# Kernel tuning notes

Hardware: AMD Instinct MI355X
Metric: run time of the kernel (lower is better)

Reference implementation:

```python
import jax, jax.numpy as jnp
import numpy as np

GRID = (128, 128, 128)
NUM_EMB = GRID[0] * GRID[1] * GRID[2]
EMB_DIM = 32
N_PTS = 2097152


def setup_inputs() -> dict:
    key = jax.random.key(0)
    k1, k2 = jax.random.split(key)
    # points uniform in the unit bounding box [0,1)^3
    x = jax.random.uniform(k1, (N_PTS, 3), dtype=jnp.float32)
    emb = jax.random.normal(k2, (NUM_EMB, EMB_DIM), dtype=jnp.float32)
    return {"x": x, "emb": emb}


def reference(x, emb):
    gx, gy, gz = GRID
    box_min = jnp.zeros((3,), jnp.float32)
    # scale_factor = grid_size / (box_max - box_min); box = [0,1]^3
    scale = jnp.array([gx, gy, gz], jnp.float32)
    xr = (x - box_min) * scale          # [N,3]
    x_idx = jnp.floor(xr)
    xw = xr - x_idx                      # trilinear weights, [N,3]

    c000 = (x_idx[:, 0] + x_idx[:, 1] * gx + x_idx[:, 2] * gx * gy).astype(jnp.int32)
    c001 = c000 + 1
    c010 = c000 + gx
    c100 = c000 + gx * gy
    c011 = c000 + gx + 1
    c101 = c000 + gx * gy + 1
    c110 = c000 + gx * gy + gx
    c111 = c000 + gx * gy + gx + 1

    # boundary clamping exactly as in the torch module
    c000 = jnp.where(c000 >= NUM_EMB, NUM_EMB - 1, c000)
    clamp = lambda c: jnp.where(c >= NUM_EMB, c000, c)
    c001, c010, c100 = clamp(c001), clamp(c010), clamp(c100)
    c011, c101, c110, c111 = clamp(c011), clamp(c101), clamp(c110), clamp(c111)

    # 8 gathers: [8, N, D]
    idx = jnp.stack([c000, c001, c010, c100, c011, c101, c110, c111])
    v = emb[idx]
    v000, v001, v010, v100, v011, v101, v110, v111 = v

    xw0 = xw[:, 0:1]
    xw1 = xw[:, 1:2]
    xw2 = xw[:, 2:3]
    c00 = v000 * (1 - xw0) + v100 * xw0
    c01 = v001 * (1 - xw0) + v101 * xw0
    c10 = v010 * (1 - xw0) + v110 * xw0
    c11 = v011 * (1 - xw0) + v111 * xw0
    c0 = c00 * (1 - xw1) + c10 * xw1
    c1 = c01 * (1 - xw1) + c11 * xw1
    return c0 * (1 - xw2) + c1 * xw2     # [N, D]
```

## Files before the change

kernel.cpp:

```cpp
#include <hip/hip_runtime.h>

#define GX 128
#define NUM_EMB (GX * GX * GX)

__global__ __launch_bounds__(256) void grid_emb_kernel(
    const float* __restrict__ x,
    const float4* __restrict__ emb4,
    float4* __restrict__ out4,
    int n_pts)
{
    int tid = blockIdx.x * 256 + threadIdx.x;
    int p = tid >> 3;
    int g = tid & 7;
    if (p >= n_pts) return;

    float xr0 = x[3 * p + 0] * (float)GX;
    float xr1 = x[3 * p + 1] * (float)GX;
    float xr2 = x[3 * p + 2] * (float)GX;
    float f0 = floorf(xr0), f1 = floorf(xr1), f2 = floorf(xr2);
    float w0 = xr0 - f0, w1 = xr1 - f1, w2 = xr2 - f2;

    int c000 = (int)f0 + (int)f1 * GX + (int)f2 * (GX * GX);
    if (c000 >= NUM_EMB) c000 = NUM_EMB - 1;

    int c[8];
    c[0] = c000;
    c[1] = c000 + 1;
    c[2] = c000 + GX;
    c[3] = c000 + GX * GX;
    c[4] = c000 + GX + 1;
    c[5] = c000 + GX * GX + 1;
    c[6] = c000 + GX * GX + GX;
    c[7] = c000 + GX * GX + GX + 1;
#pragma unroll
    for (int k = 1; k < 8; ++k) c[k] = (c[k] >= NUM_EMB) ? c000 : c[k];

    float m0 = 1.f - w0, m1 = 1.f - w1, m2 = 1.f - w2;
    float wt[8];
    wt[0] = m0 * m1 * m2;
    wt[1] = m0 * m1 * w2;
    wt[2] = m0 * w1 * m2;
    wt[3] = w0 * m1 * m2;
    wt[4] = m0 * w1 * w2;
    wt[5] = w0 * m1 * w2;
    wt[6] = w0 * w1 * m2;
    wt[7] = w0 * w1 * w2;

    float4 v[8];
#pragma unroll
    for (int k = 0; k < 8; ++k) v[k] = emb4[c[k] * 8 + g];

    float4 acc;
    acc.x = 0.f; acc.y = 0.f; acc.z = 0.f; acc.w = 0.f;
#pragma unroll
    for (int k = 0; k < 8; ++k) {
        acc.x = fmaf(wt[k], v[k].x, acc.x);
        acc.y = fmaf(wt[k], v[k].y, acc.y);
        acc.z = fmaf(wt[k], v[k].z, acc.z);
        acc.w = fmaf(wt[k], v[k].w, acc.w);
    }

    out4[p * 8 + g] = acc;
}

extern "C" void kernel_launch(void* const* d_in, const int* in_sizes, int n_in,
                              void* d_out, int out_size, void* d_ws, size_t ws_size,
                              hipStream_t stream) {
    const float* x = (const float*)d_in[0];
    const float4* emb4 = (const float4*)d_in[1];
    float4* out4 = (float4*)d_out;

    int n_pts = in_sizes[0] / 3;
    int total_threads = n_pts * 8;
    int blocks = (total_threads + 255) / 256;
    grid_emb_kernel<<<blocks, 256, 0, stream>>>(x, emb4, out4, n_pts);
}
```

Before: 684.2 us.

## Counting-sort points by grid row before trilinear gather for cache locality

Adds a histogram, scan and scatter pipeline that buckets points by their (y,z) grid row. The main kernel then processes points in that bucket order through an index indirection. Neighbouring threads gather nearby embedding rows, which should raise cache hit rates on the 256MB table that random gathers were thrashing. In exchange it adds four extra launches, atomic contention on the buckets, and scattered output writes.

```diff
diff --git a/kernel.cpp b/kernel.cpp
--- a/kernel.cpp
+++ b/kernel.cpp
@@ -2,17 +2,75 @@
 
 #define GX 128
 #define NUM_EMB (GX * GX * GX)
+#define NBUCKETS 16384
 
-__global__ __launch_bounds__(256) void grid_emb_kernel(
+
+__device__ __forceinline__ int cell_of(const float* __restrict__ x, int p) {
+    float xr0 = x[3 * p + 0] * (float)GX;
+    float xr1 = x[3 * p + 1] * (float)GX;
+    float xr2 = x[3 * p + 2] * (float)GX;
+    int i0 = (int)floorf(xr0);
+    int i1 = (int)floorf(xr1);
+    int i2 = (int)floorf(xr2);
+    int c = i0 + (i1 << 7) + (i2 << 14);
+    if (c >= NUM_EMB) c = NUM_EMB - 1;
+    return c;
+}
+
+__global__ void zero_hist_kernel(unsigned* __restrict__ hist) {
+    int i = blockIdx.x * 256 + threadIdx.x;
+    if (i < NBUCKETS) hist[i] = 0u;
+}
+
+__global__ void hist_kernel(const float* __restrict__ x, unsigned* __restrict__ hist, int n) {
+    int p = blockIdx.x * 256 + threadIdx.x;
+    if (p >= n) return;
+    atomicAdd(&hist[cell_of(x, p) >> 7], 1u);
+}
+
+__global__ __launch_bounds__(1024) void scan_kernel(unsigned* __restrict__ hist) {
+    __shared__ unsigned part[1024];
+    unsigned t = threadIdx.x;
+    unsigned base = t * 16;
+    unsigned v[16];
+    unsigned s = 0;
+#pragma unroll
+    for (int i = 0; i < 16; ++i) { v[i] = hist[base + i]; s += v[i]; }
+    part[t] = s;
+    __syncthreads();
+    for (int off = 1; off < 1024; off <<= 1) {
+        unsigned cur = part[t];
+        unsigned add = (t >= (unsigned)off) ? part[t - off] : 0u;
+        __syncthreads();
+        part[t] = cur + add;
+        __syncthreads();
+    }
+    unsigned excl = (t == 0) ? 0u : part[t - 1];
+#pragma unroll
+    for (int i = 0; i < 16; ++i) { unsigned tmp = v[i]; hist[base + i] = excl; excl += tmp; }
+}
+
+__global__ void scatter_kernel(const float* __restrict__ x, unsigned* __restrict__ cursors,
+                               unsigned* __restrict__ sorted, int n) {
+    int p = blockIdx.x * 256 + threadIdx.x;
+    if (p >= n) return;
+    unsigned b = (unsigned)(cell_of(x, p) >> 7);
+    unsigned pos = atomicAdd(&cursors[b], 1u);
+    sorted[pos] = (unsigned)p;
+}
+
+__global__ __launch_bounds__(256) void grid_emb_main_kernel(
     const float* __restrict__ x,
     const float4* __restrict__ emb4,
+    const unsigned* __restrict__ sorted,
     float4* __restrict__ out4,
     int n_pts)
 {
     int tid = blockIdx.x * 256 + threadIdx.x;
-    int p = tid >> 3;
+    int i = tid >> 3;
     int g = tid & 7;
-    if (p >= n_pts) return;
+    if (i >= n_pts) return;
+    int p = (int)sorted[i];
 
     float xr0 = x[3 * p + 0] * (float)GX;
     float xr1 = x[3 * p + 1] * (float)GX;
@@ -20,7 +78,7 @@
     float f0 = floorf(xr0), f1 = floorf(xr1), f2 = floorf(xr2);
     float w0 = xr0 - f0, w1 = xr1 - f1, w2 = xr2 - f2;
 
-    int c000 = (int)f0 + (int)f1 * GX + (int)f2 * (GX * GX);
+    int c000 = (int)f0 + ((int)f1 << 7) + ((int)f2 << 14);
     if (c000 >= NUM_EMB) c000 = NUM_EMB - 1;
 
     int c[8];
@@ -71,7 +129,18 @@
     float4* out4 = (float4*)d_out;
 
     int n_pts = in_sizes[0] / 3;
+
+    unsigned* hist = (unsigned*)d_ws;
+    unsigned* sorted = (unsigned*)((char*)d_ws + 65536);
+
+    int pblocks = (n_pts + 255) / 256;
+
+    zero_hist_kernel<<<(NBUCKETS + 255) / 256, 256, 0, stream>>>(hist);
+    hist_kernel<<<pblocks, 256, 0, stream>>>(x, hist, n_pts);
+    scan_kernel<<<1, 1024, 0, stream>>>(hist);
+    scatter_kernel<<<pblocks, 256, 0, stream>>>(x, hist, sorted, n_pts);
+
     int total_threads = n_pts * 8;
-    int blocks = (total_threads + 255) / 256;
-    grid_emb_kernel<<<blocks, 256, 0, stream>>>(x, emb4, out4, n_pts);
+    grid_emb_main_kernel<<<(total_threads + 255) / 256, 256, 0, stream>>>(
+        x, emb4, sorted, out4, n_pts);
 }
```

Measured after the change: 757.5 us. 1.11x slower.
